# Kernel optimization log

Hardware: AMD Instinct MI355X
Metric: run time of the kernel (lower is better)

## Reference

```python
import jax, jax.numpy as jnp
import numpy as np

S = 16   # num_states
C = 8    # input_channels
B = 64   # batch
L = 4096 # sequence length


def hyperbolic_sigmoid(x):
    return x / (1 + jnp.abs(x)) * 0.5 + 0.5


def hyperbolic_softmax(logits, axis):
    x = hyperbolic_sigmoid(logits)
    return x / jnp.sum(x, axis=axis, keepdims=True)


def setup_inputs() -> dict:
    key = jax.random.key(0)
    k0, k1, k2, k3 = jax.random.split(key, 4)
    return {
        "log_input_probs": jax.random.normal(k0, (B, L, C), dtype=jnp.float32),
        "invh_initial_state_probs": jax.random.normal(k1, (S,), dtype=jnp.float32),
        "invh_transition_probs": jax.random.normal(k2, (S, C, S), dtype=jnp.float32),
        "invh_accepting_state_probs": jax.random.normal(k3, (S,), dtype=jnp.float32),
    }


def reference(log_input_probs, invh_initial_state_probs, invh_transition_probs, invh_accepting_state_probs):
    # hyperbolic parameterization -> probabilities
    initial_state_probs = hyperbolic_softmax(invh_initial_state_probs, axis=0)         # (S,)
    transition_probs = hyperbolic_softmax(invh_transition_probs, axis=2)               # (S,C,S)
    accepting_state_logprobs = jnp.log(hyperbolic_sigmoid(invh_accepting_state_probs)) # (S,)

    input_probs = jnp.exp(log_input_probs)  # (B,L,C)
    # per-timestep transition matrices, (B,L,S,S)
    trans_each = jnp.einsum('pcn,blc->blpn', transition_probs, input_probs)
    # log-depth chain product m0 @ m1 @ ... @ m_{L-1} via associative scan
    prefix = jax.lax.associative_scan(jnp.matmul, trans_each, axis=1)
    transition_overall = prefix[:, -1]  # (B,S,S)
    # p_state[b,n] = sum_p overall[b,p,n] * init[p]
    p_state = jnp.einsum('bpn,p->bn', transition_overall, initial_state_probs)
    log_p_state = jnp.log(p_state + 1e-20)
    log_acceptance = jax.nn.logsumexp(log_p_state + accepting_state_logprobs[None, :], axis=1)  # (B,)
    return log_acceptance[None]  # (1,B)
```

## Files before the change

kernel.cpp:

```cpp
#include <hip/hip_runtime.h>
#include <hip/hip_bf16.h>
#include <math.h>

#define S 16
#define C 8
#define NB 64
#define L 4096
#define K 64
#define LC 64
#define NP 32

#define SLOT 324
#define RS 20
#define XSS 10

typedef __attribute__((ext_vector_type(8))) short bf16x8;
typedef __attribute__((ext_vector_type(4))) short bf16x4;
typedef __attribute__((ext_vector_type(4))) float f32x4;
typedef unsigned long long ull;

#define WS_INIT 0
#define WS_ACC  64
#define WS_CLOG 512
#define WS_TTT  16896
#define WS_CP   49664

__device__ __forceinline__ float hsig(float x) {
    return x / (1.0f + fabsf(x)) * 0.5f + 0.5f;
}
__device__ __forceinline__ unsigned int f2bf2(float a, float b) {
    __hip_bfloat162 h = __float22bfloat162_rn(make_float2(a, b));
    unsigned int u; __builtin_memcpy(&u, &h, 4); return u;
}
__device__ __forceinline__ unsigned short f2bf(float f) {
    __hip_bfloat16 h = __float2bfloat16(f);
    unsigned short u; __builtin_memcpy(&u, &h, 2); return u;
}

__device__ __forceinline__ f32x4 mfma16(bf16x4 a, bf16x4 b, f32x4 c) {
#if __has_builtin(__builtin_amdgcn_mfma_f32_16x16x16bf16_1k)
    return __builtin_amdgcn_mfma_f32_16x16x16bf16_1k(a, b, c, 0, 0, 0);
#else
    bf16x8 a8 = {a[0], a[1], a[2], a[3], 0, 0, 0, 0};
    bf16x8 b8 = {b[0], b[1], b[2], b[3], 0, 0, 0, 0};
    return __builtin_amdgcn_mfma_f32_16x16x32_bf16(a8, b8, c, 0, 0, 0);
#endif
}

__device__ __forceinline__ bf16x4 ldfrag4(const unsigned short* base, int lane) {
    return *(const bf16x4*)(base + (lane & 15) * RS + (lane >> 4) * 4);
}
__device__ __forceinline__ bf16x4 ldfrag_g4(const unsigned short* base, int lane) {
    return *(const bf16x4*)(base + (lane & 15) * 16 + (lane >> 4) * 4);
}
__device__ __forceinline__ bf16x4 cvt4(f32x4 d) {
    union { unsigned int u[2]; bf16x4 v; } cv;
    cv.u[0] = f2bf2(d[0], d[1]);
    cv.u[1] = f2bf2(d[2], d[3]);
    return cv.v;
}
__device__ __forceinline__ void store16(unsigned short* slot, f32x4 d, int lane, bool odd) {
    int col = lane & 15, quad = lane >> 4;
    if (odd) {
        ull pk = (ull)f2bf2(d[0], d[1]) | ((ull)f2bf2(d[2], d[3]) << 32);
        *(ull*)(slot + col * RS + quad * 4) = pk;
    } else {
#pragma unroll
        for (int r = 0; r < 4; r++) slot[(quad * 4 + r) * RS + col] = f2bf(d[r]);
    }
}

__device__ __forceinline__ f32x4 tree_upper(unsigned short* slots, int lane, int w,
                                            bf16x4 B1a, bf16x4 B1b) {
    f32x4 z = {0.f, 0.f, 0.f, 0.f};
    f32x4 dA = mfma16(ldfrag4(slots + (8 * w) * SLOT, lane), B1a, z);
    store16(slots + (8 * w) * SLOT, dA, lane, false);
    f32x4 dB = mfma16(ldfrag4(slots + (8 * w + 4) * SLOT, lane), B1b, z);
    f32x4 d3 = mfma16(ldfrag4(slots + (8 * w) * SLOT, lane), cvt4(dB), z);
    store16(slots + (8 * w) * SLOT, d3, lane, w & 1);
    __syncthreads();
    f32x4 root = z;
    if (w == 0) {
        f32x4 d4a = mfma16(ldfrag4(slots, lane), ldfrag4(slots + 8 * SLOT, lane), z);
        f32x4 d4b = mfma16(ldfrag4(slots + 16 * SLOT, lane), ldfrag4(slots + 24 * SLOT, lane), z);
        store16(slots, d4a, lane, false);
        root = mfma16(ldfrag4(slots, lane), cvt4(d4b), z);
    }
    return root;
}

__global__ void __launch_bounds__(256) prepall_kernel(const float* __restrict__ invh_init,
                                                      const float* __restrict__ invh_T,
                                                      const float* __restrict__ invh_acc,
                                                      unsigned char* __restrict__ wsb) {
    __shared__ float Tn[2048];
    int t = threadIdx.x;
    int cc = blockIdx.x, c = cc >> 3, c2 = cc & 7;
    if (t < S * C) {
        float v[S]; float s = 0.f;
#pragma unroll
        for (int n = 0; n < S; n++) { v[n] = hsig(invh_T[t * S + n]); s += v[n]; }
        float inv = 1.f / s;
#pragma unroll
        for (int n = 0; n < S; n++) Tn[t * S + n] = v[n] * inv;
    }
    __syncthreads();
    int p = t >> 4, n = t & 15;
    float a = 0.f;
#pragma unroll
    for (int k = 0; k < S; k++) a += Tn[(p * 8 + c) * 16 + k] * Tn[(k * 8 + c2) * 16 + n];
    ((unsigned short*)(wsb + WS_TTT))[t * 64 + cc] = f2bf(a);

    if (cc == 0 && t < S) {
        float s = 0.f;
#pragma unroll
        for (int k = 0; k < S; k++) s += hsig(invh_init[k]);
        ((float*)(wsb + WS_INIT))[t] = hsig(invh_init[t]) / s;
        ((float*)(wsb + WS_ACC))[t] = logf(hsig(invh_acc[t]));
    }
}

__global__ void __launch_bounds__(256) chunk_kernel(const float* __restrict__ logx,
                                                    unsigned char* __restrict__ wsb) {
    __shared__ __align__(16) unsigned short slots[32 * SLOT];
    __shared__ __align__(16) float xs[LC * XSS];
    __shared__ float clpart[4];

    int tid = threadIdx.x, lane = tid & 63, w = tid >> 6;
    int col = lane & 15, quad = lane >> 4;
    int pi = blockIdx.x, b = blockIdx.y;
    int chunk0 = 2 * pi;

    const unsigned short* TTT = (const unsigned short*)(wsb + WS_TTT);
    bf16x8 bfr[4][2];
#pragma unroll
    for (int jj = 0; jj < 4; jj++) {
        int t = 4 * w + jj;
#pragma unroll
        for (int kk = 0; kk < 2; kk++)
            bfr[jj][kk] = *(const bf16x8*)(TTT + (t * 16 + col) * 64 + kk * 32 + quad * 8);
    }

    const float* xg = logx + ((size_t)b * L + (size_t)chunk0 * LC) * C;
    float2 vv[2];
    vv[0] = *(const float2*)(xg + 2 * tid);
    vv[1] = *(const float2*)(xg + LC * C + 2 * tid);

    f32x4 root0, root1;
#pragma unroll
    for (int ch = 0; ch < 2; ch++) {
        int chunk = chunk0 + ch;

        float2 v = vv[ch];
        float m = fmaxf(v.x, v.y);
        m = fmaxf(m, __shfl_xor(m, 1));
        m = fmaxf(m, __shfl_xor(m, 2));
        float e0 = __expf(v.x - m), e1 = __expf(v.y - m);
        float s = e0 + e1;
        s += __shfl_xor(s, 1);
        s += __shfl_xor(s, 2);
        float inv = 1.0f / s;
        *(float2*)(xs + (tid >> 2) * XSS + 2 * (tid & 3)) = make_float2(e0 * inv, e1 * inv);
        float lx = ((tid & 3) == 0) ? (m + __logf(s)) : 0.f;
#pragma unroll
        for (int d = 1; d < 64; d <<= 1) lx += __shfl_xor(lx, d);
        if (lane == 0) clpart[w] = lx;
        __syncthreads();
        if (tid == 0)
            ((float*)(wsb + WS_CLOG))[b * K + chunk] = clpart[0] + clpart[1] + clpart[2] + clpart[3];

        bf16x8 afr[2][2];
#pragma unroll
        for (int mt = 0; mt < 2; mt++) {
            int i2 = 2 * (mt * 16 + col);
            const float2* x1p = (const float2*)(xs + (i2 + 1) * XSS);
            float2 q0 = x1p[0], q1 = x1p[1], q2 = x1p[2], q3 = x1p[3];
#pragma unroll
            for (int kk = 0; kk < 2; kk++) {
                float x0 = xs[i2 * XSS + kk * 4 + quad];
                union { unsigned int u[4]; bf16x8 v8; } cv;
                cv.u[0] = f2bf2(x0 * q0.x, x0 * q0.y);
                cv.u[1] = f2bf2(x0 * q1.x, x0 * q1.y);
                cv.u[2] = f2bf2(x0 * q2.x, x0 * q2.y);
                cv.u[3] = f2bf2(x0 * q3.x, x0 * q3.y);
                afr[mt][kk] = cv.v8;
            }
        }

#pragma unroll
        for (int mt = 0; mt < 2; mt++)
#pragma unroll
            for (int jj = 0; jj < 4; jj++) {
                f32x4 acc = {0.f, 0.f, 0.f, 0.f};
#pragma unroll
                for (int kk = 0; kk < 2; kk++)
                    acc = __builtin_amdgcn_mfma_f32_16x16x32_bf16(afr[mt][kk], bfr[jj][kk], acc, 0, 0, 0);
                int t = 4 * w + jj;
#pragma unroll
                for (int r = 0; r < 4; r++) {
                    int i = mt * 16 + quad * 4 + r;
                    int off = (i & 1) ? (col * RS + t) : (t * RS + col);
                    slots[i * SLOT + off] = f2bf(acc[r]);
                }
            }
        __syncthreads();

        bf16x4 B1[2];
        {
            f32x4 z = {0.f, 0.f, 0.f, 0.f};
#pragma unroll
            for (int i2 = 0; i2 < 4; i2++) {
                int i = 4 * w + i2;
                f32x4 d = mfma16(ldfrag4(slots + (2 * i) * SLOT, lane),
                                 ldfrag4(slots + (2 * i + 1) * SLOT, lane), z);
                if (i2 & 1) B1[i2 >> 1] = cvt4(d);
                else store16(slots + (2 * i) * SLOT, d, lane, false);
            }
        }
        f32x4 root = tree_upper(slots, lane, w, B1[0], B1[1]);
        if (ch == 0) root0 = root; else root1 = root;
    }

    if (w == 0) {
        f32x4 z = {0.f, 0.f, 0.f, 0.f};
        store16(slots, root0, lane, false);
        f32x4 fin = mfma16(ldfrag4(slots, lane), cvt4(root1), z);
        unsigned short* cp = (unsigned short*)(wsb + WS_CP) + ((size_t)b * NP + pi) * 256;
        if (pi & 1) {
            ull pk = (ull)f2bf2(fin[0], fin[1]) | ((ull)f2bf2(fin[2], fin[3]) << 32);
            *(ull*)(cp + col * 16 + quad * 4) = pk;
        } else {
#pragma unroll
            for (int r = 0; r < 4; r++) cp[(quad * 4 + r) * 16 + col] = f2bf(fin[r]);
        }
    }
}

__global__ void __launch_bounds__(256) reduce_kernel(unsigned char* __restrict__ wsb,
                                                     float* __restrict__ out) {
    __shared__ __align__(16) unsigned short slots[32 * SLOT];
    int tid = threadIdx.x, lane = tid & 63, w = tid >> 6;
    int col = lane & 15, quad = lane >> 4;
    int b = blockIdx.x;

    const unsigned short* cpb = (const unsigned short*)(wsb + WS_CP) + (size_t)b * NP * 256;
    bf16x4 B1r[2];
    {
        f32x4 z = {0.f, 0.f, 0.f, 0.f};
#pragma unroll
        for (int i2 = 0; i2 < 4; i2++) {
            int i = 4 * w + i2;
            f32x4 d = mfma16(ldfrag_g4(cpb + (size_t)(2 * i) * 256, lane),
                             ldfrag_g4(cpb + (size_t)(2 * i + 1) * 256, lane), z);
            if (i2 & 1) B1r[i2 >> 1] = cvt4(d);
            else store16(slots + (2 * i) * SLOT, d, lane, false);
        }
    }
    f32x4 troot = tree_upper(slots, lane, w, B1r[0], B1r[1]);

    if (w == 0) {
        const float* initp = (const float*)(wsb + WS_INIT);
        const float* acclog = (const float*)(wsb + WS_ACC);
        float part = 0.f;
#pragma unroll
        for (int r = 0; r < 4; r++) part += initp[quad * 4 + r] * troot[r];
        part += __shfl_xor(part, 16);
        part += __shfl_xor(part, 32);
        float lp = logf(fmaxf(part, 0.f) + 1e-30f) + acclog[col];
        float mx = lp;
#pragma unroll
        for (int d = 1; d < 16; d <<= 1) mx = fmaxf(mx, __shfl_xor(mx, d));
        float a2 = isfinite(mx) ? mx : 0.0f;
        float sm = expf(lp - a2);
#pragma unroll
        for (int d = 1; d < 16; d <<= 1) sm += __shfl_xor(sm, d);
        float cl = ((const float*)(wsb + WS_CLOG))[b * K + lane];
#pragma unroll
        for (int d = 1; d < 64; d <<= 1) cl += __shfl_xor(cl, d);
        if (lane == 0) out[b] = logf(sm) + a2 + cl;
    }
}

extern "C" void kernel_launch(void* const* d_in, const int* in_sizes, int n_in,
                              void* d_out, int out_size, void* d_ws, size_t ws_size,
                              hipStream_t stream) {
    const float* logx = (const float*)d_in[0];
    const float* init = (const float*)d_in[1];
    const float* T    = (const float*)d_in[2];
    const float* acc  = (const float*)d_in[3];
    unsigned char* wsb = (unsigned char*)d_ws;
    float* out = (float*)d_out;

    prepall_kernel<<<64, 256, 0, stream>>>(init, T, acc, wsb);
    chunk_kernel<<<dim3(K / 2, NB), 256, 0, stream>>>(logx, wsb);
    reduce_kernel<<<NB, 256, 0, stream>>>(wsb, out);
}
```

Baseline: 83.26 us.

## Fuse parameter preparation into chunk and reduce kernels, drop prep launch

Removes the separate prep kernel. Each chunk block now normalizes the transition tensor into shared memory and computes its own slice of the paired-transition products (T_c·T_c2) as bf16 fragments in registers. The reduce kernel computes the initial and accepting probabilities inline. This saves one kernel launch and the global workspace round trip. In exchange, all 2048 chunk blocks redundantly compute about 16x8x16 FMAs per thread, plus an extra shared-memory sync.

```diff
diff --git a/kernel.cpp b/kernel.cpp
--- a/kernel.cpp
+++ b/kernel.cpp
@@ -19,11 +19,8 @@
 typedef __attribute__((ext_vector_type(4))) float f32x4;
 typedef unsigned long long ull;
 
-#define WS_INIT 0
-#define WS_ACC  64
-#define WS_CLOG 512
-#define WS_TTT  16896
-#define WS_CP   49664
+#define WS_CLOG 0
+#define WS_CP   16384
 
 __device__ __forceinline__ float hsig(float x) {
     return x / (1.0f + fabsf(x)) * 0.5f + 0.5f;
@@ -89,40 +86,10 @@
     return root;
 }
 
-__global__ void __launch_bounds__(256) prepall_kernel(const float* __restrict__ invh_init,
-                                                      const float* __restrict__ invh_T,
-                                                      const float* __restrict__ invh_acc,
-                                                      unsigned char* __restrict__ wsb) {
-    __shared__ float Tn[2048];
-    int t = threadIdx.x;
-    int cc = blockIdx.x, c = cc >> 3, c2 = cc & 7;
-    if (t < S * C) {
-        float v[S]; float s = 0.f;
-#pragma unroll
-        for (int n = 0; n < S; n++) { v[n] = hsig(invh_T[t * S + n]); s += v[n]; }
-        float inv = 1.f / s;
-#pragma unroll
-        for (int n = 0; n < S; n++) Tn[t * S + n] = v[n] * inv;
-    }
-    __syncthreads();
-    int p = t >> 4, n = t & 15;
-    float a = 0.f;
-#pragma unroll
-    for (int k = 0; k < S; k++) a += Tn[(p * 8 + c) * 16 + k] * Tn[(k * 8 + c2) * 16 + n];
-    ((unsigned short*)(wsb + WS_TTT))[t * 64 + cc] = f2bf(a);
-
-    if (cc == 0 && t < S) {
-        float s = 0.f;
-#pragma unroll
-        for (int k = 0; k < S; k++) s += hsig(invh_init[k]);
-        ((float*)(wsb + WS_INIT))[t] = hsig(invh_init[t]) / s;
-        ((float*)(wsb + WS_ACC))[t] = logf(hsig(invh_acc[t]));
-    }
-}
-
 __global__ void __launch_bounds__(256) chunk_kernel(const float* __restrict__ logx,
+                                                    const float* __restrict__ invh_T,
                                                     unsigned char* __restrict__ wsb) {
-    __shared__ __align__(16) unsigned short slots[32 * SLOT];
+    __shared__ __align__(16) unsigned char smem[32 * SLOT * 2];
     __shared__ __align__(16) float xs[LC * XSS];
     __shared__ float clpart[4];
 
@@ -131,21 +98,60 @@
     int pi = blockIdx.x, b = blockIdx.y;
     int chunk0 = 2 * pi;
 
-    const unsigned short* TTT = (const unsigned short*)(wsb + WS_TTT);
-    bf16x8 bfr[4][2];
-#pragma unroll
-    for (int jj = 0; jj < 4; jj++) {
-        int t = 4 * w + jj;
-#pragma unroll
-        for (int kk = 0; kk < 2; kk++)
-            bfr[jj][kk] = *(const bf16x8*)(TTT + (t * 16 + col) * 64 + kk * 32 + quad * 8);
-    }
-
     const float* xg = logx + ((size_t)b * L + (size_t)chunk0 * LC) * C;
     float2 vv[2];
     vv[0] = *(const float2*)(xg + 2 * tid);
     vv[1] = *(const float2*)(xg + LC * C + 2 * tid);
 
+    float* TnL = (float*)smem;
+    {
+        const float4* tg = (const float4*)invh_T + tid * 2;
+        float4 aa = tg[0], bb = tg[1];
+        float va[8] = {aa.x, aa.y, aa.z, aa.w, bb.x, bb.y, bb.z, bb.w};
+        float s = 0.f;
+#pragma unroll
+        for (int i = 0; i < 8; i++) { va[i] = hsig(va[i]); s += va[i]; }
+        s += __shfl_xor(s, 1);
+        float inv = 1.f / s;
+        float4 o0 = {va[0] * inv, va[1] * inv, va[2] * inv, va[3] * inv};
+        float4 o1 = {va[4] * inv, va[5] * inv, va[6] * inv, va[7] * inv};
+        ((float4*)TnL)[tid * 2] = o0;
+        ((float4*)TnL)[tid * 2 + 1] = o1;
+    }
+    __syncthreads();
+
+    bf16x8 bfr[4][2];
+#pragma unroll
+    for (int kk = 0; kk < 2; kk++) {
+        float acc[4][8];
+#pragma unroll
+        for (int jj = 0; jj < 4; jj++)
+#pragma unroll
+            for (int j = 0; j < 8; j++) acc[jj][j] = 0.f;
+#pragma unroll
+        for (int k = 0; k < 16; k++) {
+            float bc[8];
+#pragma unroll
+            for (int j = 0; j < 8; j++) bc[j] = TnL[(k * 8 + j) * 16 + col];
+#pragma unroll
+            for (int jj = 0; jj < 4; jj++) {
+                float ar = TnL[((4 * w + jj) * 8 + kk * 4 + quad) * 16 + k];
+#pragma unroll
+                for (int j = 0; j < 8; j++) acc[jj][j] += ar * bc[j];
+            }
+        }
+#pragma unroll
+        for (int jj = 0; jj < 4; jj++) {
+            union { unsigned int u[4]; bf16x8 v8; } cv;
+            cv.u[0] = f2bf2(acc[jj][0], acc[jj][1]);
+            cv.u[1] = f2bf2(acc[jj][2], acc[jj][3]);
+            cv.u[2] = f2bf2(acc[jj][4], acc[jj][5]);
+            cv.u[3] = f2bf2(acc[jj][6], acc[jj][7]);
+            bfr[jj][kk] = cv.v8;
+        }
+    }
+
+    unsigned short* slots = (unsigned short*)smem;
     f32x4 root0, root1;
 #pragma unroll
     for (int ch = 0; ch < 2; ch++) {
@@ -237,6 +243,8 @@
 }
 
 __global__ void __launch_bounds__(256) reduce_kernel(unsigned char* __restrict__ wsb,
+                                                     const float* __restrict__ invh_init,
+                                                     const float* __restrict__ invh_acc,
                                                      float* __restrict__ out) {
     __shared__ __align__(16) unsigned short slots[32 * SLOT];
     int tid = threadIdx.x, lane = tid & 63, w = tid >> 6;
@@ -259,14 +267,16 @@
     f32x4 troot = tree_upper(slots, lane, w, B1r[0], B1r[1]);
 
     if (w == 0) {
-        const float* initp = (const float*)(wsb + WS_INIT);
-        const float* acclog = (const float*)(wsb + WS_ACC);
+        float si = 0.f;
+#pragma unroll
+        for (int k = 0; k < S; k++) si += hsig(invh_init[k]);
+        float isi = 1.f / si;
         float part = 0.f;
 #pragma unroll
-        for (int r = 0; r < 4; r++) part += initp[quad * 4 + r] * troot[r];
+        for (int r = 0; r < 4; r++) part += hsig(invh_init[quad * 4 + r]) * isi * troot[r];
         part += __shfl_xor(part, 16);
         part += __shfl_xor(part, 32);
-        float lp = logf(fmaxf(part, 0.f) + 1e-30f) + acclog[col];
+        float lp = logf(fmaxf(part, 0.f) + 1e-30f) + logf(hsig(invh_acc[col]));
         float mx = lp;
 #pragma unroll
         for (int d = 1; d < 16; d <<= 1) mx = fmaxf(mx, __shfl_xor(mx, d));
@@ -291,7 +301,6 @@
     unsigned char* wsb = (unsigned char*)d_ws;
     float* out = (float*)d_out;
 
-    prepall_kernel<<<64, 256, 0, stream>>>(init, T, acc, wsb);
-    chunk_kernel<<<dim3(K / 2, NB), 256, 0, stream>>>(logx, wsb);
-    reduce_kernel<<<NB, 256, 0, stream>>>(wsb, out);
-}
+    chunk_kernel<<<dim3(NP, NB), 256, 0, stream>>>(logx, T, wsb);
+    reduce_kernel<<<NB, 256, 0, stream>>>(wsb, init, acc, out);
+}
```

Measured after the change: 116.3 us. +39.7%, slower.

## Process four chunks per block and shrink the reduction tree input

Applied to the files above, without the earlier changes.

Each chunk_kernel block now handles four 64-step chunks instead of two and combines them with three extra 16x16 MFMA products before writing one partial matrix. The grid halves to 16x64 blocks, and reduce_kernel receives 16 partial matrices per batch, so its first MFMA level is replaced by direct fragment loads into LDS. SLOT padding also changes from 324 to 320. This lowers the number of blocks and the amount of reduction work, but each block has a longer serial chain and the GPU gets less parallelism (1024 blocks).

```diff
diff --git a/kernel.cpp b/kernel.cpp
--- a/kernel.cpp
+++ b/kernel.cpp
@@ -8,9 +8,9 @@
 #define L 4096
 #define K 64
 #define LC 64
-#define NP 32
-
-#define SLOT 324
+#define NQ 16
+
+#define SLOT 320
 #define RS 20
 #define XSS 10
 
@@ -128,8 +128,8 @@
 
     int tid = threadIdx.x, lane = tid & 63, w = tid >> 6;
     int col = lane & 15, quad = lane >> 4;
-    int pi = blockIdx.x, b = blockIdx.y;
-    int chunk0 = 2 * pi;
+    int qi = blockIdx.x, b = blockIdx.y;
+    int chunk0 = 4 * qi;
 
     const unsigned short* TTT = (const unsigned short*)(wsb + WS_TTT);
     bf16x8 bfr[4][2];
@@ -142,16 +142,17 @@
     }
 
     const float* xg = logx + ((size_t)b * L + (size_t)chunk0 * LC) * C;
-    float2 vv[2];
-    vv[0] = *(const float2*)(xg + 2 * tid);
-    vv[1] = *(const float2*)(xg + LC * C + 2 * tid);
-
-    f32x4 root0, root1;
-#pragma unroll
-    for (int ch = 0; ch < 2; ch++) {
+    float2 vv0 = *(const float2*)(xg + 2 * tid);
+    float2 vv1 = *(const float2*)(xg + 1 * LC * C + 2 * tid);
+    float2 vv2 = *(const float2*)(xg + 2 * LC * C + 2 * tid);
+    float2 vv3 = *(const float2*)(xg + 3 * LC * C + 2 * tid);
+
+    f32x4 r0, r1, r2, r3;
+#pragma unroll
+    for (int ch = 0; ch < 4; ch++) {
         int chunk = chunk0 + ch;
 
-        float2 v = vv[ch];
+        float2 v = (ch == 0) ? vv0 : (ch == 1) ? vv1 : (ch == 2) ? vv2 : vv3;
         float m = fmaxf(v.x, v.y);
         m = fmaxf(m, __shfl_xor(m, 1));
         m = fmaxf(m, __shfl_xor(m, 2));
@@ -218,15 +219,20 @@
             }
         }
         f32x4 root = tree_upper(slots, lane, w, B1[0], B1[1]);
-        if (ch == 0) root0 = root; else root1 = root;
+        if (ch == 0) r0 = root; else if (ch == 1) r1 = root;
+        else if (ch == 2) r2 = root; else r3 = root;
     }
 
     if (w == 0) {
         f32x4 z = {0.f, 0.f, 0.f, 0.f};
-        store16(slots, root0, lane, false);
-        f32x4 fin = mfma16(ldfrag4(slots, lane), cvt4(root1), z);
-        unsigned short* cp = (unsigned short*)(wsb + WS_CP) + ((size_t)b * NP + pi) * 256;
-        if (pi & 1) {
+        store16(slots, r0, lane, false);
+        f32x4 p01 = mfma16(ldfrag4(slots, lane), cvt4(r1), z);
+        store16(slots + 8 * SLOT, r2, lane, false);
+        f32x4 p23 = mfma16(ldfrag4(slots + 8 * SLOT, lane), cvt4(r3), z);
+        store16(slots, p01, lane, false);
+        f32x4 fin = mfma16(ldfrag4(slots, lane), cvt4(p23), z);
+        unsigned short* cp = (unsigned short*)(wsb + WS_CP) + ((size_t)b * NQ + qi) * 256;
+        if (qi & 1) {
             ull pk = (ull)f2bf2(fin[0], fin[1]) | ((ull)f2bf2(fin[2], fin[3]) << 32);
             *(ull*)(cp + col * 16 + quad * 4) = pk;
         } else {
@@ -243,20 +249,14 @@
     int col = lane & 15, quad = lane >> 4;
     int b = blockIdx.x;
 
-    const unsigned short* cpb = (const unsigned short*)(wsb + WS_CP) + (size_t)b * NP * 256;
-    bf16x4 B1r[2];
-    {
-        f32x4 z = {0.f, 0.f, 0.f, 0.f};
-#pragma unroll
-        for (int i2 = 0; i2 < 4; i2++) {
-            int i = 4 * w + i2;
-            f32x4 d = mfma16(ldfrag_g4(cpb + (size_t)(2 * i) * 256, lane),
-                             ldfrag_g4(cpb + (size_t)(2 * i + 1) * 256, lane), z);
-            if (i2 & 1) B1r[i2 >> 1] = cvt4(d);
-            else store16(slots + (2 * i) * SLOT, d, lane, false);
-        }
-    }
-    f32x4 troot = tree_upper(slots, lane, w, B1r[0], B1r[1]);
+    const unsigned short* cpb = (const unsigned short*)(wsb + WS_CP) + (size_t)b * NQ * 256;
+    bf16x4 e0 = ldfrag_g4(cpb + (size_t)(4 * w + 0) * 256, lane);
+    bf16x4 e1 = ldfrag_g4(cpb + (size_t)(4 * w + 2) * 256, lane);
+    bf16x4 B1a = ldfrag_g4(cpb + (size_t)(4 * w + 1) * 256, lane);
+    bf16x4 B1b = ldfrag_g4(cpb + (size_t)(4 * w + 3) * 256, lane);
+    *(bf16x4*)(slots + (8 * w) * SLOT + col * RS + quad * 4) = e0;
+    *(bf16x4*)(slots + (8 * w + 4) * SLOT + col * RS + quad * 4) = e1;
+    f32x4 troot = tree_upper(slots, lane, w, B1a, B1b);
 
     if (w == 0) {
         const float* initp = (const float*)(wsb + WS_INIT);
@@ -292,6 +292,6 @@
     float* out = (float*)d_out;
 
     prepall_kernel<<<64, 256, 0, stream>>>(init, T, acc, wsb);
-    chunk_kernel<<<dim3(K / 2, NB), 256, 0, stream>>>(logx, wsb);
+    chunk_kernel<<<dim3(NQ, NB), 256, 0, stream>>>(logx, wsb);
     reduce_kernel<<<NB, 256, 0, stream>>>(wsb, out);
 }
```

Measured after the change: 81.67 us, median of 2. Within noise of the previous version (-1.9%).
